# Kernel tuning notes

Measured on AMD Instinct MI355X. Metric: run time of the kernel, lower is better.

## Reference

```python
import jax, jax.numpy as jnp
import numpy as np

# Module hyperparameters (init_kwargs): shape_data = [n_t, n_y, n_x]
N_T, N_Y, N_X = 5, 32, 32
N = N_Y * N_X            # nb_nodes
DX = DY = DT = 1.0


def setup_inputs() -> dict:
    key = jax.random.key(0)
    k1, k2, k3 = jax.random.split(key, 3)
    n_b = 4
    kappa = jax.random.uniform(k1, (n_b, 1, N, N_T), dtype=jnp.float32)
    m = jax.random.normal(k2, (n_b, 2, N, N_T), dtype=jnp.float32)
    H = jax.random.normal(k3, (n_b, 2, 2, N, N_T), dtype=jnp.float32)
    return {"kappa": kappa, "m": m, "H": H}


def _stencil_indices():
    # 9-point stencil on the n_y x n_x grid; row-major node index = y*n_x + x.
    yy, xx = np.meshgrid(np.arange(N_Y), np.arange(N_X), indexing="ij")
    yy, xx = yy.reshape(-1), xx.reshape(-1)
    node = np.arange(N)
    offs = [(0, 0), (0, 1), (0, -1), (1, 0), (-1, 0), (1, 1), (1, -1), (-1, 1), (-1, -1)]
    rows, cols, valid = [], [], []
    for oy, ox in offs:
        ny, nx = yy + oy, xx + ox
        ok = (ny >= 0) & (ny < N_Y) & (nx >= 0) & (nx < N_X)
        rows.append(node)
        cols.append(np.where(ok, ny * N_X + nx, node))
        valid.append(ok.astype(np.float32))
    return (jnp.asarray(np.concatenate(rows)),
            jnp.asarray(np.concatenate(cols)),
            jnp.asarray(np.concatenate(valid)))

ROWS, COLS, VALID = _stencil_indices()


def _build_A(kappa, m, H):
    # Finite-difference discretization of A = kappa^2 I + m.grad - div(H grad)
    # kappa: [b,t,N]; m: [b,t,2,N]; H: [b,t,2,2,N]
    mx, my = m[..., 0, :], m[..., 1, :]
    H11, H22 = H[..., 0, 0, :], H[..., 1, 1, :]
    H12 = 0.5 * (H[..., 0, 1, :] + H[..., 1, 0, :])
    c0 = kappa ** 2 + 2.0 * H11 / DX ** 2 + 2.0 * H22 / DY ** 2   # center
    cpx = mx / (2 * DX) - H11 / DX ** 2                           # (0,+1)
    cmx = -mx / (2 * DX) - H11 / DX ** 2                          # (0,-1)
    cpy = my / (2 * DY) - H22 / DY ** 2                           # (+1,0)
    cmy = -my / (2 * DY) - H22 / DY ** 2                          # (-1,0)
    cc = H12 / (2 * DX * DY)                                      # cross term
    # order matches _stencil_indices offsets
    vals = jnp.concatenate([c0, cpx, cmx, cpy, cmy, -cc, cc, cc, -cc], axis=-1)
    vals = vals * VALID                                           # zero out-of-grid neighbors
    b, t = vals.shape[0], vals.shape[1]
    A = jnp.zeros((b, t, N, N), vals.dtype)
    return A.at[:, :, ROWS, COLS].add(vals)


def reference(kappa, m, H):
    # rearrange to [batch, time, ...] leading
    kap = jnp.transpose(kappa[:, 0], (0, 2, 1))          # [b,t,N]
    mm = jnp.transpose(m, (0, 3, 1, 2))                  # [b,t,2,N]
    HH = jnp.transpose(H, (0, 4, 1, 2, 3))               # [b,t,2,2,N]
    A = _build_A(kap, mm, HH)                            # [b,t,N,N]
    I = jnp.eye(N, dtype=A.dtype)
    M = I + DT * A                                       # M_k = Id + dt * A_k
    MM = jnp.einsum("btij,btjk->btik", M, M)             # spspmm(M_k, M_k)
    b = M.shape[0]
    Q = jnp.zeros((b, N_T * N, N_T * N), A.dtype)
    # block-tridiagonal precision matrix assembly (QR = Id)
    Q = Q.at[:, 0:N, 0:N].set(MM[:, 0])
    Q = Q.at[:, 0:N, N:2 * N].set(-M[:, 1])
    for i in range(1, N_T - 1):
        Q = Q.at[:, i * N:(i + 1) * N, (i - 1) * N:i * N].set(-M[:, i - 1])
        Q = Q.at[:, i * N:(i + 1) * N, i * N:(i + 1) * N].set(MM[:, i] + I)
        Q = Q.at[:, i * N:(i + 1) * N, (i + 1) * N:(i + 2) * N].set(-M[:, i + 1])
    i = N_T - 1
    Q = Q.at[:, i * N:(i + 1) * N, (i - 1) * N:i * N].set(-M[:, i - 1])
    Q = Q.at[:, i * N:(i + 1) * N, i * N:(i + 1) * N].set(MM[:, i])
    return Q
```

## Files before the change

kernel.cpp:

```cpp
#include <hip/hip_runtime.h>

#define NT   5
#define NY   32
#define NX   32
#define NN   1024
#define QDIM 5120
#define NB   4
#define G    8

typedef float vfloat4 __attribute__((ext_vector_type(4)));

__device__ const int c_oy[9] = {0, 0, 0, 1, -1, 1, 1, -1, -1};
__device__ const int c_ox[9] = {0, 1, -1, 0, 0, 1, -1, 1, -1};

__device__ __forceinline__ void stencil9(const float* __restrict__ kap,
                                         const float* __restrict__ m,
                                         const float* __restrict__ H,
                                         int b, int t, int n, float s[9]) {
    float k   = kap[((size_t)b * NN + n) * NT + t];
    float mx  = m[(((size_t)b * 2 + 0) * NN + n) * NT + t];
    float my  = m[(((size_t)b * 2 + 1) * NN + n) * NT + t];
    float H11 = H[((((size_t)b * 2 + 0) * 2 + 0) * NN + n) * NT + t];
    float H01 = H[((((size_t)b * 2 + 0) * 2 + 1) * NN + n) * NT + t];
    float H10 = H[((((size_t)b * 2 + 1) * 2 + 0) * NN + n) * NT + t];
    float H22 = H[((((size_t)b * 2 + 1) * 2 + 1) * NN + n) * NT + t];
    float cc = 0.25f * (H01 + H10);
    s[0] = 1.0f + k * k + 2.0f * H11 + 2.0f * H22;
    s[1] =  0.5f * mx - H11;
    s[2] = -0.5f * mx - H11;
    s[3] =  0.5f * my - H22;
    s[4] = -0.5f * my - H22;
    s[5] = -cc;
    s[6] =  cc;
    s[7] =  cc;
    s[8] = -cc;
    int y = n >> 5, x = n & 31;
    if (x == NX - 1) { s[1] = 0.f; s[5] = 0.f; s[7] = 0.f; }
    if (x == 0)      { s[2] = 0.f; s[6] = 0.f; s[8] = 0.f; }
    if (y == NY - 1) { s[3] = 0.f; s[5] = 0.f; s[6] = 0.f; }
    if (y == 0)      { s[4] = 0.f; s[7] = 0.f; s[8] = 0.f; }
}

__global__ __launch_bounds__(256) void spde_fused_g8p(const float* __restrict__ kap,
                                                      const float* __restrict__ m,
                                                      const float* __restrict__ H,
                                                      float* __restrict__ Q) {
    const int oy[9] = {0, 0, 0, 1, -1, 1, 1, -1, -1};
    const int ox[9] = {0, 1, -1, 0, 0, 1, -1, 1, -1};

    int blk = blockIdx.x;
    int b   = blk / (NT * (NN / G));
    int rem = blk - b * (NT * (NN / G));
    int t   = rem >> 7;
    int grp = rem & 127;
    int base = grp << 3;
    int ry = base >> 5;
    int rxb = base & 31;
    int tid = threadIdx.x;

    __shared__ float band[G * 3 * 5 * 32];
    __shared__ float sk[G][9][9];
    __shared__ float moff[G][2][9];

    {
        vfloat4 z4 = {0.f, 0.f, 0.f, 0.f};
        vfloat4* p = (vfloat4*)band;
#pragma unroll
        for (int w = 0; w < 4; ++w) {
            int idx = tid + 256 * w;
            if (idx < (G * 3 * 5 * 32) / 4) p[idx] = z4;
        }
    }
    if (tid < G * 11) {
        int j = tid / 11, u = tid - j * 11;
        int rj = base + j;
        if (u < 9) {
            int ky = ry + c_oy[u], kx = (rxb + j) + c_ox[u];
            bool valid = ((unsigned)ky < NY) && ((unsigned)kx < NX);
            int k = valid ? (ky * NX + kx) : rj;
            float s[9];
            stencil9(kap, m, H, b, t, k, s);
#pragma unroll
            for (int e = 0; e < 9; ++e)
                sk[j][u][(oy[e] + 1) * 3 + (ox[e] + 1)] = s[e];
        } else if (u == 9) {
            float s[9] = {0, 0, 0, 0, 0, 0, 0, 0, 0};
            if (t >= 1) stencil9(kap, m, H, b, t - 1, rj, s);
#pragma unroll
            for (int e = 0; e < 9; ++e) moff[j][0][e] = -s[e];
        } else {
            float s[9] = {0, 0, 0, 0, 0, 0, 0, 0, 0};
            if (t <= NT - 2) stencil9(kap, m, H, b, t + 1, rj, s);
#pragma unroll
            for (int e = 0; e < 9; ++e) moff[j][1][e] = -s[e];
        }
    }
    __syncthreads();

    for (int it = tid; it < G * 43; it += 256) {
        int j = it / 43, q = it - j * 43;
        int rxj = rxb + j;
        if (q < 25) {
            int dy = q / 5 - 2, dx = q % 5 - 2;
            float a = 0.f;
#pragma unroll
            for (int d1 = 0; d1 < 9; ++d1) {
                int dy2 = dy - oy[d1], dx2 = dx - ox[d1];
                if (dy2 >= -1 && dy2 <= 1 && dx2 >= -1 && dx2 <= 1) {
                    a += sk[j][0][(oy[d1] + 1) * 3 + (ox[d1] + 1)]
                       * sk[j][d1][(dy2 + 1) * 3 + (dx2 + 1)];
                }
            }
            if (q == 12 && t >= 1 && t <= NT - 2) a += 1.0f;
            int cy = ry + dy, cx = rxj + dx;
            if ((unsigned)cy < NY && (unsigned)cx < NX)
                band[((j * 3 + 1) * 5 + (dy + 2)) * 32 + cx] = a;
        } else if (q < 34) {
            int d = q - 25;
            int cy = ry + c_oy[d], cx = rxj + c_ox[d];
            if ((unsigned)cy < NY && (unsigned)cx < NX)
                band[((j * 3 + 0) * 5 + (c_oy[d] + 2)) * 32 + cx] = moff[j][0][d];
        } else {
            int d = q - 34;
            int cy = ry + c_oy[d], cx = rxj + c_ox[d];
            if ((unsigned)cy < NY && (unsigned)cx < NX)
                band[((j * 3 + 2) * 5 + (c_oy[d] + 2)) * 32 + cx] = moff[j][1][d];
        }
    }
    __syncthreads();

    int cy  = tid >> 3;
    int cx4 = (tid & 7) * 4;
    int br  = cy - (ry - 2);
    bool inband = (unsigned)br < 5u;
    int br_c = inband ? br : 0;
    const float* bp = band + br_c * 32 + cx4;
    float* dst = Q + ((size_t)b * QDIM + (size_t)t * NN + base) * QDIM + 4 * tid;
    vfloat4 z4 = {0.f, 0.f, 0.f, 0.f};
#pragma unroll
    for (int j = 0; j < G; ++j) {
#pragma unroll
        for (int kk = 0; kk < NT; ++kk) {
            int z = kk - t + 1;
            bool ok = ((unsigned)z < 3u) && inband;
            int z_c = ((unsigned)z < 3u) ? z : 0;
            vfloat4 v = ok ? *(const vfloat4*)(bp + (j * 3 + z_c) * 160) : z4;
            *(vfloat4*)(dst + (size_t)j * QDIM + kk * NN) = v;
        }
    }
}

extern "C" void kernel_launch(void* const* d_in, const int* in_sizes, int n_in,
                              void* d_out, int out_size, void* d_ws, size_t ws_size,
                              hipStream_t stream) {
    const float* kap = (const float*)d_in[0];
    const float* m   = (const float*)d_in[1];
    const float* H   = (const float*)d_in[2];
    float* Q = (float*)d_out;

    int nblocks = NB * NT * (NN / G);
    spde_fused_g8p<<<nblocks, 256, 0, stream>>>(kap, m, H, Q);
}
```

Measured before the change: 423.9 us.

## Split fused kernel into band-build and grid-stride Q streaming kernels

The fused kernel is split in two. The first kernel builds each row group's compact 3x5x32 band in shared memory and writes it to a workspace buffer. The second kernel is a grid-stride streaming pass that writes the whole dense Q with coalesced vector stores, gathering the nonzero band values from the workspace. The aim is to decouple the costly dense write of mostly zeros from the stencil product work and get closer to peak write bandwidth. In exchange it adds an extra workspace round trip of about 39 MB and a second launch. The fallback path, used when no workspace is available, reads the band back from the same buffer it is overwriting, so it is unsafe.

```diff
diff --git a/kernel.cpp b/kernel.cpp
--- a/kernel.cpp
+++ b/kernel.cpp
@@ -41,10 +41,10 @@
     if (y == 0)      { s[4] = 0.f; s[7] = 0.f; s[8] = 0.f; }
 }
 
-__global__ __launch_bounds__(256) void spde_fused_g8p(const float* __restrict__ kap,
-                                                      const float* __restrict__ m,
-                                                      const float* __restrict__ H,
-                                                      float* __restrict__ Q) {
+__global__ __launch_bounds__(256) void spde_band_build(const float* __restrict__ kap,
+                                                       const float* __restrict__ m,
+                                                       const float* __restrict__ H,
+                                                       float* __restrict__ ws) {
     const int oy[9] = {0, 0, 0, 1, -1, 1, 1, -1, -1};
     const int ox[9] = {0, 1, -1, 0, 0, 1, -1, 1, -1};
 
@@ -129,24 +129,43 @@
     }
     __syncthreads();
 
-    int cy  = tid >> 3;
-    int cx4 = (tid & 7) * 4;
-    int br  = cy - (ry - 2);
-    bool inband = (unsigned)br < 5u;
-    int br_c = inband ? br : 0;
-    const float* bp = band + br_c * 32 + cx4;
-    float* dst = Q + ((size_t)b * QDIM + (size_t)t * NN + base) * QDIM + 4 * tid;
-    vfloat4 z4 = {0.f, 0.f, 0.f, 0.f};
+    {
+        size_t rowbase = (size_t)((b * NT + t) * NN + base);
+        vfloat4* dst = (vfloat4*)(ws + rowbase * 480);
+        const vfloat4* src = (const vfloat4*)band;
 #pragma unroll
-    for (int j = 0; j < G; ++j) {
-#pragma unroll
-        for (int kk = 0; kk < NT; ++kk) {
-            int z = kk - t + 1;
-            bool ok = ((unsigned)z < 3u) && inband;
-            int z_c = ((unsigned)z < 3u) ? z : 0;
-            vfloat4 v = ok ? *(const vfloat4*)(bp + (j * 3 + z_c) * 160) : z4;
-            *(vfloat4*)(dst + (size_t)j * QDIM + kk * NN) = v;
+        for (int w = 0; w < 4; ++w) {
+            int idx = tid + 256 * w;
+            if (idx < 960) dst[idx] = src[idx];
         }
+    }
+}
+
+__global__ __launch_bounds__(256) void spde_stream(const float* __restrict__ ws,
+                                                   float* __restrict__ Q) {
+    const unsigned total4 = (unsigned)NB * QDIM * (QDIM / 4);
+    unsigned p = blockIdx.x * 256u + threadIdx.x;
+    const unsigned stride = gridDim.x * 256u;
+    const vfloat4 z4 = {0.f, 0.f, 0.f, 0.f};
+    const vfloat4* ws4 = (const vfloat4*)ws;
+    vfloat4* Q4 = (vfloat4*)Q;
+    for (; p < total4; p += stride) {
+        unsigned row  = p / 1280u;
+        unsigned col4 = p - row * 1280u;
+        int t  = (int)((row >> 10) % 5u);
+        int ry = (int)((row >> 5) & 31u);
+        int kk = (int)(col4 >> 8);
+        int c4 = (int)(col4 & 255u);
+        int cy = c4 >> 3, cxq = c4 & 7;
+        int z  = kk - t + 1;
+        int dy = cy - ry + 2;
+        vfloat4 v = z4;
+        if ((unsigned)z < 3u) {
+            int dc = min(max(dy, 0), 4);
+            vfloat4 w = ws4[(size_t)row * 120 + (z * 5 + dc) * 8 + cxq];
+            v = ((unsigned)dy < 5u) ? w : z4;
+        }
+        Q4[p] = v;
     }
 }
 
@@ -158,6 +177,15 @@
     const float* H   = (const float*)d_in[2];
     float* Q = (float*)d_out;
 
-    int nblocks = NB * NT * (NN / G);
-    spde_fused_g8p<<<nblocks, 256, 0, stream>>>(kap, m, H, Q);
+    const size_t ws_needed = (size_t)NB * NT * NN * 480 * sizeof(float);
+    if (d_ws != nullptr && ws_size >= ws_needed) {
+        float* ws = (float*)d_ws;
+        int nblocks = NB * NT * (NN / G);
+        spde_band_build<<<nblocks, 256, 0, stream>>>(kap, m, H, ws);
+        spde_stream<<<4096, 256, 0, stream>>>(ws, Q);
+    } else {
+        int nblocks = NB * NT * (NN / G);
+        spde_band_build<<<nblocks, 256, 0, stream>>>(kap, m, H, (float*)d_out);
+        spde_stream<<<4096, 256, 0, stream>>>((const float*)d_out, Q);
+    }
 }
```

New measurement: 450.5 us. +6.3%, slower.

## Zero output with memset and store only the nonzero band blocks

Applied to the files above, without the earlier changes.

The whole dense Q is now zeroed with hipMemsetAsync, and the fused kernel writes only the nonzero stencil band: three time blocks and five grid rows per output row. Previously every thread stored a vfloat4 for every column of the dense 5120x5120 output, zeros included. The intent is to let the runtime's fill path handle the bulk zero traffic and keep the kernel's global stores to the sparse band. The cost is an extra operation on the stream, and the band region is written twice. Correctness assumes out_size is given in bytes.

```diff
diff --git a/kernel.cpp b/kernel.cpp
--- a/kernel.cpp
+++ b/kernel.cpp
@@ -41,10 +41,10 @@
     if (y == 0)      { s[4] = 0.f; s[7] = 0.f; s[8] = 0.f; }
 }
 
-__global__ __launch_bounds__(256) void spde_fused_g8p(const float* __restrict__ kap,
-                                                      const float* __restrict__ m,
-                                                      const float* __restrict__ H,
-                                                      float* __restrict__ Q) {
+__global__ __launch_bounds__(256) void spde_band_sparse(const float* __restrict__ kap,
+                                                        const float* __restrict__ m,
+                                                        const float* __restrict__ H,
+                                                        float* __restrict__ Q) {
     const int oy[9] = {0, 0, 0, 1, -1, 1, 1, -1, -1};
     const int ox[9] = {0, 1, -1, 0, 0, 1, -1, 1, -1};
 
@@ -129,23 +129,24 @@
     }
     __syncthreads();
 
-    int cy  = tid >> 3;
-    int cx4 = (tid & 7) * 4;
-    int br  = cy - (ry - 2);
-    bool inband = (unsigned)br < 5u;
-    int br_c = inband ? br : 0;
-    const float* bp = band + br_c * 32 + cx4;
-    float* dst = Q + ((size_t)b * QDIM + (size_t)t * NN + base) * QDIM + 4 * tid;
-    vfloat4 z4 = {0.f, 0.f, 0.f, 0.f};
 #pragma unroll
-    for (int j = 0; j < G; ++j) {
-#pragma unroll
-        for (int kk = 0; kk < NT; ++kk) {
-            int z = kk - t + 1;
-            bool ok = ((unsigned)z < 3u) && inband;
-            int z_c = ((unsigned)z < 3u) ? z : 0;
-            vfloat4 v = ok ? *(const vfloat4*)(bp + (j * 3 + z_c) * 160) : z4;
-            *(vfloat4*)(dst + (size_t)j * QDIM + kk * NN) = v;
+    for (int w = 0; w < 4; ++w) {
+        int idx = tid + 256 * w;
+        if (idx < 960) {
+            int j   = idx / 120;
+            int rm  = idx - j * 120;
+            int z   = rm / 40;
+            int rm2 = rm - z * 40;
+            int dr  = rm2 >> 3;
+            int cxq = rm2 & 7;
+            int kk = t - 1 + z;
+            int cy = ry - 2 + dr;
+            if ((unsigned)kk < (unsigned)NT && (unsigned)cy < (unsigned)NY) {
+                vfloat4 v = *(const vfloat4*)&band[((j * 3 + z) * 5 + dr) * 32 + cxq * 4];
+                size_t off = ((size_t)b * QDIM + (size_t)t * NN + base + j) * QDIM
+                           + (size_t)kk * NN + cy * 32 + cxq * 4;
+                *(vfloat4*)(Q + off) = v;
+            }
         }
     }
 }
@@ -158,6 +159,8 @@
     const float* H   = (const float*)d_in[2];
     float* Q = (float*)d_out;
 
+    hipMemsetAsync(d_out, 0, (size_t)out_size, stream);
+
     int nblocks = NB * NT * (NN / G);
-    spde_fused_g8p<<<nblocks, 256, 0, stream>>>(kap, m, H, Q);
+    spde_band_sparse<<<nblocks, 256, 0, stream>>>(kap, m, H, Q);
 }
```

Result: faster. 365.3 us (-13.8%).
